# Optimization experiments

Measured on AMD Instinct MI355X. Metric: run time of the kernel, lower is better.

## Reference

```python
import jax, jax.numpy as jnp
import numpy as np

PC_RANGE = np.array([-20.0, -20.0, -2.3, 20.0, 20.0, 0.9], np.float32)
GRID = np.array([0.1, 0.1, 0.1], np.float32)
K = 5                      # kernel_size
C_IN, C_OUT = 128, 128
BS, G = 8, 2000
SPATIAL = tuple(int(s) for s in ((PC_RANGE[3:] - PC_RANGE[:3]) / GRID).astype(np.int32))  # (400,400,32)


def setup_inputs() -> dict:
    key = jax.random.key(0)
    k1, k2, k3 = jax.random.split(key, 3)
    instance_feature = jax.random.normal(k1, (BS, G, C_IN), jnp.float32)
    anchor = jax.random.uniform(k2, (BS, G, 3), jnp.float32)          # normalized xyz in [0,1)
    w = jax.random.normal(k3, (K ** 3, C_IN, C_OUT), jnp.float32) * 0.02  # SubMConv3d weight, flattened offsets
    return {"instance_feature": instance_feature, "anchor": anchor, "w": w}


def _voxel_indices(anchor):
    # cartesian(): map normalized anchor xyz into the pc_range box, then voxelize.
    lo = jnp.asarray(PC_RANGE[:3])
    hi = jnp.asarray(PC_RANGE[3:])
    xyz = anchor[..., :3] * (hi - lo) + lo                 # [bs, g, 3]
    idx = ((xyz - lo) / jnp.asarray(GRID)).astype(jnp.int32)
    return idx


def reference(instance_feature, anchor, w):
    bs, g, c = instance_feature.shape
    n = bs * g
    idx = _voxel_indices(anchor).reshape(n, 3)             # [n, 3] int32 voxel coords
    bidx = jnp.repeat(jnp.arange(bs, dtype=jnp.int32), g)  # [n]
    Dx, Dy, Dz = SPATIAL

    # Rulebook substitute: dense voxel -> point-id lookup (-1 = inactive).
    grid = jnp.full((bs, Dx, Dy, Dz), -1, jnp.int32)
    grid = grid.at[bidx, idx[:, 0], idx[:, 1], idx[:, 2]].set(jnp.arange(n, dtype=jnp.int32))

    feats = instance_feature.reshape(n, c)
    r = (K - 1) // 2
    ax = jnp.arange(-r, r + 1, dtype=jnp.int32)
    offs = jnp.stack(jnp.meshgrid(ax, ax, ax, indexing="ij"), -1).reshape(-1, 3)  # [K^3, 3]
    dims = jnp.asarray([Dx, Dy, Dz], jnp.int32)

    # Submanifold conv: gather neighbor features per kernel offset, matmul, accumulate.
    def step(acc, inp):
        off, wk = inp                                       # off [3], wk [Cin, Cout]
        nb = idx + off[None, :]                             # [n, 3]
        inb = jnp.all((nb >= 0) & (nb < dims[None, :]), axis=-1)
        nbc = jnp.clip(nb, 0, dims[None, :] - 1)
        j = grid[bidx, nbc[:, 0], nbc[:, 1], nbc[:, 2]]     # [n] neighbor point id or -1
        valid = inb & (j >= 0)
        fj = jnp.where(valid[:, None], feats[jnp.clip(j, 0, n - 1)], 0.0)  # [n, Cin]
        return acc + fj @ wk, None

    out0 = jnp.zeros((n, C_OUT), feats.dtype)
    out, _ = jax.lax.scan(step, out0, (offs, w))
    return out.reshape(bs, g, C_OUT)                        # output_proj = Identity
```

## Files before the change

kernel.cpp:

```cpp
#include <hip/hip_runtime.h>
#include <stdint.h>

#define BSZ 8
#define GQ 2000
#define NPTS (BSZ * GQ)
#define CH 128
#define KOFF 125
#define KSELF 62
#define TBL_BITS 16
#define TBL_SIZE (1 << TBL_BITS)
#define TBL_MASK (TBL_SIZE - 1)
#define OTHER_CAP 16384
#define TM 32
#define AS_LD 129

#define WS_CNT_OFF   524288
#define WS_P62_OFF   524544
#define WS_POTH_OFF  589056
#define WS_VOX_OFF   851200

struct Slot { int key; int val; };

__device__ __forceinline__ uint32_t hash_of(uint32_t k) {
    return (k * 2654435761u) >> (32 - TBL_BITS);
}

__device__ __forceinline__ int3 voxel_idx(const float* __restrict__ anchor, int i,
                                          float sx, float sy, float sz,
                                          float lx, float ly, float lz, float g) {
    float ax = anchor[i * 3 + 0];
    float ay = anchor[i * 3 + 1];
    float az = anchor[i * 3 + 2];
    float x = __fadd_rn(__fmul_rn(ax, sx), lx);
    float y = __fadd_rn(__fmul_rn(ay, sy), ly);
    float z = __fadd_rn(__fmul_rn(az, sz), lz);
    int ix = (int)__fdiv_rn(__fsub_rn(x, lx), g);
    int iy = (int)__fdiv_rn(__fsub_rn(y, ly), g);
    int iz = (int)__fdiv_rn(__fsub_rn(z, lz), g);
    return make_int3(ix, iy, iz);
}

__global__ void build_hash_kernel(const float* __restrict__ anchor,
                                  Slot* __restrict__ tab,
                                  int4* __restrict__ voxbuf,
                                  int* __restrict__ counters,
                                  float sx, float sy, float sz,
                                  float lx, float ly, float lz, float g,
                                  int Dx, int Dy, int Dz) {
    int i = blockIdx.x * blockDim.x + threadIdx.x;
    if (i == 0) counters[0] = 0;
    if (i >= NPTS) return;
    int3 v = voxel_idx(anchor, i, sx, sy, sz, lx, ly, lz, g);
    int b = i / GQ;
    voxbuf[i] = make_int4(v.x, v.y, v.z, b);
    if (v.x < 0 || v.x >= Dx || v.y < 0 || v.y >= Dy || v.z < 0 || v.z >= Dz) return;
    int key = ((b * Dx + v.x) * Dy + v.y) * Dz + v.z;
    uint32_t slot = hash_of((uint32_t)key);
    for (;;) {
        int prev = atomicCAS(&tab[slot].key, -1, key);
        if (prev == -1 || prev == key) {
            atomicMax(&tab[slot].val, i);
            break;
        }
        slot = (slot + 1) & TBL_MASK;
    }
}

__device__ __forceinline__ int hash_query(const Slot* __restrict__ tab, int key) {
    uint32_t slot = hash_of((uint32_t)key);
    for (;;) {
        int k = tab[slot].key;
        if (k == key) return tab[slot].val;
        if (k == -1) return -1;
        slot = (slot + 1) & TBL_MASK;
    }
}

__global__ void pairgen_kernel(const int4* __restrict__ voxbuf,
                               const Slot* __restrict__ tab,
                               int* __restrict__ counters,
                               int* __restrict__ pairs62,
                               int4* __restrict__ pairsOther,
                               int Dx, int Dy, int Dz) {
    int tid = blockIdx.x * blockDim.x + threadIdx.x;
    bool inrange = tid < NPTS * KOFF;
    int ti = inrange ? tid : 0;
    int i = ti / KOFF;
    int k = ti - i * KOFF;
    int4 v = voxbuf[i];
    int ox = k / 25 - 2;
    int oy = (k / 5) % 5 - 2;
    int oz = k % 5 - 2;
    int nx = v.x + ox, ny = v.y + oy, nz = v.z + oz;
    bool inb = inrange && nx >= 0 && nx < Dx && ny >= 0 && ny < Dy && nz >= 0 && nz < Dz;
    int j = -1;
    if (inb) {
        int key = ((v.w * Dx + nx) * Dy + ny) * Dz + nz;
        j = hash_query(tab, key);
    }
    bool isself = inrange && (k == KSELF);
    if (isself) pairs62[i] = j;
    bool hit = inrange && !isself && (j >= 0);
    unsigned long long mask = __ballot(hit);
    if (mask) {
        int lane = threadIdx.x & 63;
        int leader = __ffsll((unsigned long long)mask) - 1;
        int cnt = __popcll(mask);
        int base = 0;
        if (lane == leader) base = atomicAdd(&counters[0], cnt);
        base = __shfl(base, leader);
        if (hit) {
            int pos = base + (int)__popcll(mask & ((1ULL << lane) - 1ULL));
            if (pos < OTHER_CAP) pairsOther[pos] = make_int4(i, j, k, 0);
        }
    }
}

__global__ void __launch_bounds__(256)
gemm62_kernel(const float* __restrict__ feat,
              const float* __restrict__ w,
              const int* __restrict__ pairs62,
              float* __restrict__ out) {
    __shared__ float As[TM * AS_LD];

    int rowbase = blockIdx.x * TM;
    int t = threadIdx.x;

    for (int f = t; f < TM * 32; f += 256) {
        int r = f >> 5;
        int c4 = f & 31;
        int j = pairs62[rowbase + r];
        float4 val = make_float4(0.f, 0.f, 0.f, 0.f);
        if (j >= 0) val = *(const float4*)(feat + (size_t)j * CH + c4 * 4);
        float* dst = As + r * AS_LD + c4 * 4;
        dst[0] = val.x; dst[1] = val.y; dst[2] = val.z; dst[3] = val.w;
    }
    __syncthreads();

    int tc = t & 31;
    int tr = t >> 5;
    int r0 = tr * 4;

    float acc[4][4];
    #pragma unroll
    for (int a = 0; a < 4; ++a)
        #pragma unroll
        for (int b = 0; b < 4; ++b) acc[a][b] = 0.f;

    const float* B = w + (size_t)KSELF * CH * CH + tc * 4;
    #pragma unroll 4
    for (int k = 0; k < CH; ++k) {
        float4 b4 = *(const float4*)(B + (size_t)k * CH);
        float a0 = As[(r0 + 0) * AS_LD + k];
        float a1 = As[(r0 + 1) * AS_LD + k];
        float a2 = As[(r0 + 2) * AS_LD + k];
        float a3 = As[(r0 + 3) * AS_LD + k];
        acc[0][0] = fmaf(a0, b4.x, acc[0][0]); acc[0][1] = fmaf(a0, b4.y, acc[0][1]);
        acc[0][2] = fmaf(a0, b4.z, acc[0][2]); acc[0][3] = fmaf(a0, b4.w, acc[0][3]);
        acc[1][0] = fmaf(a1, b4.x, acc[1][0]); acc[1][1] = fmaf(a1, b4.y, acc[1][1]);
        acc[1][2] = fmaf(a1, b4.z, acc[1][2]); acc[1][3] = fmaf(a1, b4.w, acc[1][3]);
        acc[2][0] = fmaf(a2, b4.x, acc[2][0]); acc[2][1] = fmaf(a2, b4.y, acc[2][1]);
        acc[2][2] = fmaf(a2, b4.z, acc[2][2]); acc[2][3] = fmaf(a2, b4.w, acc[2][3]);
        acc[3][0] = fmaf(a3, b4.x, acc[3][0]); acc[3][1] = fmaf(a3, b4.y, acc[3][1]);
        acc[3][2] = fmaf(a3, b4.z, acc[3][2]); acc[3][3] = fmaf(a3, b4.w, acc[3][3]);
    }

    #pragma unroll
    for (int rr = 0; rr < 4; ++rr) {
        int i = rowbase + r0 + rr;
        float4 v = make_float4(acc[rr][0], acc[rr][1], acc[rr][2], acc[rr][3]);
        *(float4*)(out + (size_t)i * CH + tc * 4) = v;
    }
}

__global__ void __launch_bounds__(CH)
scatter_other_kernel(const float* __restrict__ feat,
                     const float* __restrict__ w,
                     const int4* __restrict__ pairsOther,
                     const int* __restrict__ counters,
                     float* __restrict__ out) {
    __shared__ float fbuf[CH];
    int n = counters[0];
    if (n > OTHER_CAP) n = OTHER_CAP;
    int t = threadIdx.x;
    for (int p = blockIdx.x; p < n; p += gridDim.x) {
        int4 pr = pairsOther[p];
        __syncthreads();
        fbuf[t] = feat[(size_t)pr.y * CH + t];
        __syncthreads();
        const float* wk = w + (size_t)pr.z * CH * CH + t;
        float a0 = 0.f, a1 = 0.f, a2 = 0.f, a3 = 0.f;
        #pragma unroll 8
        for (int c = 0; c < CH; c += 4) {
            a0 = fmaf(fbuf[c + 0], wk[(c + 0) * CH], a0);
            a1 = fmaf(fbuf[c + 1], wk[(c + 1) * CH], a1);
            a2 = fmaf(fbuf[c + 2], wk[(c + 2) * CH], a2);
            a3 = fmaf(fbuf[c + 3], wk[(c + 3) * CH], a3);
        }
        atomicAdd(&out[(size_t)pr.x * CH + t], (a0 + a1) + (a2 + a3));
    }
}

extern "C" void kernel_launch(void* const* d_in, const int* in_sizes, int n_in,
                              void* d_out, int out_size, void* d_ws, size_t ws_size,
                              hipStream_t stream) {
    const float* feat   = (const float*)d_in[0];
    const float* anchor = (const float*)d_in[1];
    const float* w      = (const float*)d_in[2];
    float* out = (float*)d_out;

    char* ws = (char*)d_ws;
    Slot* tab        = (Slot*)ws;
    int*  counters   = (int*)(ws + WS_CNT_OFF);
    int*  pairs62    = (int*)(ws + WS_P62_OFF);
    int4* pairsOther = (int4*)(ws + WS_POTH_OFF);
    int4* voxbuf     = (int4*)(ws + WS_VOX_OFF);

    hipMemsetAsync(tab, 0xFF, (size_t)TBL_SIZE * sizeof(Slot), stream);

    float lx = -20.0f, ly = -20.0f, lz = -2.3f;
    float hx =  20.0f, hy =  20.0f, hz =  0.9f;
    float sx = hx - lx, sy = hy - ly, sz = hz - lz;
    float g = 0.1f;
    int Dx = (int)(sx / g);
    int Dy = (int)(sy / g);
    int Dz = (int)(sz / g);

    build_hash_kernel<<<(NPTS + 255) / 256, 256, 0, stream>>>(
        anchor, tab, voxbuf, counters, sx, sy, sz, lx, ly, lz, g, Dx, Dy, Dz);

    pairgen_kernel<<<(NPTS * KOFF + 255) / 256, 256, 0, stream>>>(
        voxbuf, tab, counters, pairs62, pairsOther, Dx, Dy, Dz);

    gemm62_kernel<<<NPTS / TM, 256, 0, stream>>>(
        feat, w, pairs62, out);

    scatter_other_kernel<<<512, CH, 0, stream>>>(
        feat, w, pairsOther, counters, out);
}
```

Measured before the change: 112.1 us.

## Stage self-offset weight tiles in shared memory, shrink row tile, vectorize hash probe

The self-offset GEMM now stages the weight matrix through shared memory in 32-row chunks and halves the row tile to 16, doubling the block count. The idea is to cut redundant global weight reads and improve occupancy. The hash probe now reads key and value as one int2 load, and the scatter kernel's inner loop is unrolled further. The A-tile sync now relies on the first chunk's barrier, and each block reloads the full 64KB weight slice, so total weight traffic rises with the extra blocks.

```diff
diff --git a/kernel.cpp b/kernel.cpp
--- a/kernel.cpp
+++ b/kernel.cpp
@@ -11,8 +11,9 @@
 #define TBL_SIZE (1 << TBL_BITS)
 #define TBL_MASK (TBL_SIZE - 1)
 #define OTHER_CAP 16384
-#define TM 32
+#define TM 16
 #define AS_LD 129
+#define KB 32
 
 #define WS_CNT_OFF   524288
 #define WS_P62_OFF   524544
@@ -69,9 +70,9 @@
 __device__ __forceinline__ int hash_query(const Slot* __restrict__ tab, int key) {
     uint32_t slot = hash_of((uint32_t)key);
     for (;;) {
-        int k = tab[slot].key;
-        if (k == key) return tab[slot].val;
-        if (k == -1) return -1;
+        int2 kv = *(const int2*)(&tab[slot]);
+        if (kv.x == key) return kv.y;
+        if (kv.x == -1) return -1;
         slot = (slot + 1) & TBL_MASK;
     }
 }
@@ -122,10 +123,12 @@
               const int* __restrict__ pairs62,
               float* __restrict__ out) {
     __shared__ float As[TM * AS_LD];
+    __shared__ float Bs[KB * CH];
 
     int rowbase = blockIdx.x * TM;
     int t = threadIdx.x;
 
+    #pragma unroll
     for (int f = t; f < TM * 32; f += 256) {
         int r = f >> 5;
         int c4 = f & 31;
@@ -135,38 +138,45 @@
         float* dst = As + r * AS_LD + c4 * 4;
         dst[0] = val.x; dst[1] = val.y; dst[2] = val.z; dst[3] = val.w;
     }
-    __syncthreads();
 
     int tc = t & 31;
     int tr = t >> 5;
-    int r0 = tr * 4;
-
-    float acc[4][4];
-    #pragma unroll
-    for (int a = 0; a < 4; ++a)
+    int r0 = tr * 2;
+
+    float acc[2][4];
+    #pragma unroll
+    for (int a = 0; a < 2; ++a)
         #pragma unroll
         for (int b = 0; b < 4; ++b) acc[a][b] = 0.f;
 
-    const float* B = w + (size_t)KSELF * CH * CH + tc * 4;
-    #pragma unroll 4
-    for (int k = 0; k < CH; ++k) {
-        float4 b4 = *(const float4*)(B + (size_t)k * CH);
-        float a0 = As[(r0 + 0) * AS_LD + k];
-        float a1 = As[(r0 + 1) * AS_LD + k];
-        float a2 = As[(r0 + 2) * AS_LD + k];
-        float a3 = As[(r0 + 3) * AS_LD + k];
-        acc[0][0] = fmaf(a0, b4.x, acc[0][0]); acc[0][1] = fmaf(a0, b4.y, acc[0][1]);
-        acc[0][2] = fmaf(a0, b4.z, acc[0][2]); acc[0][3] = fmaf(a0, b4.w, acc[0][3]);
-        acc[1][0] = fmaf(a1, b4.x, acc[1][0]); acc[1][1] = fmaf(a1, b4.y, acc[1][1]);
-        acc[1][2] = fmaf(a1, b4.z, acc[1][2]); acc[1][3] = fmaf(a1, b4.w, acc[1][3]);
-        acc[2][0] = fmaf(a2, b4.x, acc[2][0]); acc[2][1] = fmaf(a2, b4.y, acc[2][1]);
-        acc[2][2] = fmaf(a2, b4.z, acc[2][2]); acc[2][3] = fmaf(a2, b4.w, acc[2][3]);
-        acc[3][0] = fmaf(a3, b4.x, acc[3][0]); acc[3][1] = fmaf(a3, b4.y, acc[3][1]);
-        acc[3][2] = fmaf(a3, b4.z, acc[3][2]); acc[3][3] = fmaf(a3, b4.w, acc[3][3]);
-    }
-
-    #pragma unroll
-    for (int rr = 0; rr < 4; ++rr) {
+    const float* B = w + (size_t)KSELF * CH * CH;
+
+    #pragma unroll
+    for (int chunk = 0; chunk < CH / KB; ++chunk) {
+        __syncthreads();
+        #pragma unroll
+        for (int f = t; f < KB * 32; f += 256) {
+            int kk = f >> 5;
+            int c4 = f & 31;
+            *(float4*)(Bs + kk * CH + c4 * 4) =
+                *(const float4*)(B + (size_t)(chunk * KB + kk) * CH + c4 * 4);
+        }
+        __syncthreads();
+
+        #pragma unroll 4
+        for (int kk = 0; kk < KB; ++kk) {
+            float4 b4 = *(const float4*)(Bs + kk * CH + tc * 4);
+            float a0 = As[(r0 + 0) * AS_LD + chunk * KB + kk];
+            float a1 = As[(r0 + 1) * AS_LD + chunk * KB + kk];
+            acc[0][0] = fmaf(a0, b4.x, acc[0][0]); acc[0][1] = fmaf(a0, b4.y, acc[0][1]);
+            acc[0][2] = fmaf(a0, b4.z, acc[0][2]); acc[0][3] = fmaf(a0, b4.w, acc[0][3]);
+            acc[1][0] = fmaf(a1, b4.x, acc[1][0]); acc[1][1] = fmaf(a1, b4.y, acc[1][1]);
+            acc[1][2] = fmaf(a1, b4.z, acc[1][2]); acc[1][3] = fmaf(a1, b4.w, acc[1][3]);
+        }
+    }
+
+    #pragma unroll
+    for (int rr = 0; rr < 2; ++rr) {
         int i = rowbase + r0 + rr;
         float4 v = make_float4(acc[rr][0], acc[rr][1], acc[rr][2], acc[rr][3]);
         *(float4*)(out + (size_t)i * CH + tc * 4) = v;
@@ -190,7 +200,7 @@
         __syncthreads();
         const float* wk = w + (size_t)pr.z * CH * CH + t;
         float a0 = 0.f, a1 = 0.f, a2 = 0.f, a3 = 0.f;
-        #pragma unroll 8
+        #pragma unroll 16
         for (int c = 0; c < CH; c += 4) {
             a0 = fmaf(fbuf[c + 0], wk[(c + 0) * CH], a0);
             a1 = fmaf(fbuf[c + 1], wk[(c + 1) * CH], a1);
```

New measurement: 112.1 us. Within noise of the previous version (+0.0%).
